# Kernel tuning notes

Measured on AMD Instinct MI355X. Metric: run time of the kernel, lower is better.

Reference implementation:

```python
import jax, jax.numpy as jnp
import numpy as np

N_NODES = 10000
N_EDGES = 160000
D = 512            # input_dim = hidden_size = output_dim
NUM_EXPERTS = 4
N_LAYERS = 2


def setup_inputs() -> dict:
    key = jax.random.key(0)
    k = jax.random.split(key, 7)
    x = jax.random.normal(k[0], (N_NODES, D), dtype=jnp.float32)
    edge_index = jax.random.randint(k[1], (2, N_EDGES), 0, N_NODES, dtype=jnp.int32)
    # Gating network (Linear D -> NUM_EXPERTS)
    gate_w = jax.random.normal(k[2], (D, NUM_EXPERTS), dtype=jnp.float32) * 0.05
    gate_b = jnp.zeros((NUM_EXPERTS,), dtype=jnp.float32)
    # Per-expert SAGEConv weights: lin_r (self/root) and lin_l (neighbor) + bias
    w_self = jax.random.normal(k[3], (NUM_EXPERTS, N_LAYERS, D, D), dtype=jnp.float32) * 0.05
    w_neigh = jax.random.normal(k[4], (NUM_EXPERTS, N_LAYERS, D, D), dtype=jnp.float32) * 0.05
    b_exp = jnp.zeros((NUM_EXPERTS, N_LAYERS, D), dtype=jnp.float32)
    return {"x": x, "edge_index": edge_index, "gate_w": gate_w, "gate_b": gate_b,
            "w_self": w_self, "w_neigh": w_neigh, "b_exp": b_exp, "top_k": 1}


def reference(x, edge_index, gate_w, gate_b, w_self, w_neigh, b_exp, top_k):
    n = x.shape[0]
    src, dst = edge_index[0], edge_index[1]
    # mean-aggregation normalization (PyG SAGEConv aggr='mean'); 0 for isolated nodes
    deg = jax.ops.segment_sum(jnp.ones_like(src, dtype=x.dtype), dst, num_segments=n)
    inv_deg = jnp.where(deg > 0, 1.0 / jnp.maximum(deg, 1.0), 0.0)[:, None]  # [N,1]

    # gating: softmax(Linear(x)) then top-k routing
    gate = jax.nn.softmax(x @ gate_w + gate_b, axis=-1)          # [N, E]
    top_vals, top_idx = jax.lax.top_k(gate, top_k)               # [N, k]

    def expert(ws, wn, b):  # ws, wn: [L, D, D]; b: [L, D]
        h = x
        for l in range(N_LAYERS):
            agg = jax.ops.segment_sum(h[src], dst, num_segments=n) * inv_deg
            # SAGEConv: lin_l(mean_neigh) + lin_r(x) + bias, then relu (norm='id', eval dropout)
            h = jax.nn.relu(agg @ wn[l] + h @ ws[l] + b[l])
        return h

    # dense all-expert compute (matches original module)
    outs = jax.vmap(expert)(w_self, w_neigh, b_exp)              # [E, N, D]
    outs = jnp.transpose(outs, (1, 0, 2))                        # [N, E, D]
    sel = jnp.take_along_axis(outs, top_idx[:, :, None], axis=1)  # [N, k, D]
    return jnp.sum(sel * top_vals[:, :, None], axis=1)           # [N, D]
```

## Files before the change

### kernel.cpp

```cpp
#include <hip/hip_runtime.h>
#include <hip/hip_bf16.h>
#include <cstdint>

#define N_NODES 10000
#define N_EDGES 160000
#define DIM 512
#define K1 1024
#define NEXP 4

typedef __bf16 bf16_t;
typedef bf16_t bf16x8 __attribute__((ext_vector_type(8)));
typedef float f32x4 __attribute__((ext_vector_type(4)));

#define AS1(p) ((__attribute__((address_space(1))) void*)(p))
#define AS3(p) ((__attribute__((address_space(3))) void*)(p))

__global__ void zero_kernel(int* __restrict__ deg, int* __restrict__ ecnt) {
    int i = blockIdx.x * blockDim.x + threadIdx.x;
    if (i < N_NODES) deg[i] = 0;
    if (i < NEXP) ecnt[i] = 0;
}

__global__ void gate_kernel(const float* __restrict__ x,
                            const float* __restrict__ gw,
                            const float* __restrict__ gb,
                            int* __restrict__ top_idx,
                            float* __restrict__ top_val,
                            bf16_t* __restrict__ acat) {
    const int wave = threadIdx.x >> 6;
    const int lane = threadIdx.x & 63;
    const int node = blockIdx.x * 4 + wave;
    if (node >= N_NODES) return;
    const float4* x4 = (const float4*)(x + (size_t)node * DIM);
    const float4* gw4 = (const float4*)gw;
    float4 xa = x4[lane * 2];
    float4 xb = x4[lane * 2 + 1];
    float xv[8] = { xa.x, xa.y, xa.z, xa.w, xb.x, xb.y, xb.z, xb.w };
    float a0 = 0.f, a1 = 0.f, a2 = 0.f, a3 = 0.f;
    #pragma unroll
    for (int c = 0; c < 8; c++) {
        float4 g = gw4[lane * 8 + c];
        a0 += xv[c] * g.x; a1 += xv[c] * g.y; a2 += xv[c] * g.z; a3 += xv[c] * g.w;
    }
    bf16x8 o;
    #pragma unroll
    for (int c = 0; c < 8; c++) o[c] = (bf16_t)xv[c];
    *(bf16x8*)(acat + (size_t)node * K1 + DIM + lane * 8) = o;
    for (int off = 32; off > 0; off >>= 1) {
        a0 += __shfl_xor(a0, off);
        a1 += __shfl_xor(a1, off);
        a2 += __shfl_xor(a2, off);
        a3 += __shfl_xor(a3, off);
    }
    if (lane == 0) {
        float z[4] = { a0 + gb[0], a1 + gb[1], a2 + gb[2], a3 + gb[3] };
        int bi = 0; float bm = z[0];
        for (int e = 1; e < 4; e++) if (z[e] > bm) { bm = z[e]; bi = e; }
        float den = 0.f;
        for (int e = 0; e < 4; e++) den += expf(z[e] - bm);
        top_idx[node] = bi;
        top_val[node] = 1.0f / den;
    }
}

__global__ void bucket_kernel(const int* __restrict__ top_idx,
                              int* __restrict__ ecnt,
                              int* __restrict__ lists) {
    __shared__ int lcnt[NEXP];
    __shared__ int base[NEXP];
    const int tid = threadIdx.x;
    if (tid < NEXP) lcnt[tid] = 0;
    __syncthreads();
    const int node = blockIdx.x * 256 + tid;
    int e = 0, rank = 0;
    if (node < N_NODES) {
        e = top_idx[node];
        rank = atomicAdd(&lcnt[e], 1);
    }
    __syncthreads();
    if (tid < NEXP) base[tid] = atomicAdd(&ecnt[tid], lcnt[tid]);
    __syncthreads();
    if (node < N_NODES) lists[e * N_NODES + base[e] + rank] = node;
}

__global__ void deg_kernel(const int* __restrict__ dst, int* __restrict__ deg) {
    int i = blockIdx.x * blockDim.x + threadIdx.x;
    if (i < N_EDGES) atomicAdd(&deg[dst[i]], 1);
}

__global__ void scan_kernel(const int* __restrict__ deg,
                            int* __restrict__ offs,
                            int* __restrict__ cursor) {
    __shared__ int wsum[16];
    __shared__ int carrysh;
    const int tid = threadIdx.x;
    const int lane = tid & 63;
    const int wv = tid >> 6;
    if (tid == 0) carrysh = 0;
    __syncthreads();
    for (int base = 0; base < N_NODES; base += 1024) {
        int i = base + tid;
        int v = (i < N_NODES) ? deg[i] : 0;
        int s = v;
        #pragma unroll
        for (int off = 1; off < 64; off <<= 1) {
            int t = __shfl_up(s, off);
            if (lane >= off) s += t;
        }
        if (lane == 63) wsum[wv] = s;
        int carry = carrysh;
        __syncthreads();
        if (wv == 0) {
            int w = (lane < 16) ? wsum[lane] : 0;
            #pragma unroll
            for (int off = 1; off < 16; off <<= 1) {
                int t = __shfl_up(w, off);
                if (lane >= off) w += t;
            }
            if (lane < 16) wsum[lane] = w;
        }
        __syncthreads();
        int wbase = (wv > 0) ? wsum[wv - 1] : 0;
        int excl = carry + wbase + s - v;
        if (i < N_NODES) { offs[i] = excl; cursor[i] = excl; }
        int total = wsum[15];
        __syncthreads();
        if (tid == 0) carrysh = carry + total;
        __syncthreads();
    }
    if (tid == 0) offs[N_NODES] = carrysh;
}

__global__ void fill_kernel(const int* __restrict__ src, const int* __restrict__ dst,
                            int* __restrict__ cursor, int* __restrict__ csr) {
    int i = blockIdx.x * blockDim.x + threadIdx.x;
    if (i < N_EDGES) {
        int d = dst[i];
        int p = atomicAdd(&cursor[d], 1);
        csr[p] = src[i];
    }
}

__global__ void wtrans_kernel(const float* __restrict__ w_neigh,
                              const float* __restrict__ w_self,
                              bf16_t* __restrict__ Bt) {
    __shared__ float tile[32][33];
    const int m = blockIdx.z;
    const bool isSelf = m >= 8;
    const int el = m & 7;
    const float* W = (isSelf ? w_self : w_neigh) + (size_t)el * DIM * DIM;
    const int k0 = blockIdx.x * 32;
    const int n0 = blockIdx.y * 32;
    const int tx = threadIdx.x, ty = threadIdx.y;
    for (int r = ty; r < 32; r += 8)
        tile[r][tx] = W[(size_t)(k0 + r) * DIM + n0 + tx];
    __syncthreads();
    for (int r = ty; r < 32; r += 8) {
        int n = n0 + r;
        int k = k0 + tx;
        Bt[((size_t)el * DIM + n) * K1 + (isSelf ? DIM : 0) + k] = (bf16_t)tile[tx][r];
    }
}

__global__ void agg1_kernel(const int* __restrict__ offs, const int* __restrict__ csr,
                            bf16_t* __restrict__ acat) {
    const int wave = threadIdx.x >> 6;
    const int lane = threadIdx.x & 63;
    const int node = blockIdx.x * 4 + wave;
    if (node >= N_NODES) return;
    const int c0 = lane * 8;
    float s[8] = {0,0,0,0,0,0,0,0};
    int beg = offs[node];
    int end = offs[node + 1];
    int d = end - beg;
    int p = beg;
    for (; p + 8 <= end; p += 8) {
        bf16x8 v[8];
        #pragma unroll
        for (int q = 0; q < 8; q++) {
            int idx = csr[p + q];
            v[q] = *(const bf16x8*)(acat + (size_t)idx * K1 + DIM + c0);
        }
        #pragma unroll
        for (int q = 0; q < 8; q++)
            #pragma unroll
            for (int k = 0; k < 8; k++) s[k] += (float)v[q][k];
    }
    for (; p + 4 <= end; p += 4) {
        bf16x8 v[4];
        #pragma unroll
        for (int q = 0; q < 4; q++) {
            int idx = csr[p + q];
            v[q] = *(const bf16x8*)(acat + (size_t)idx * K1 + DIM + c0);
        }
        #pragma unroll
        for (int q = 0; q < 4; q++)
            #pragma unroll
            for (int k = 0; k < 8; k++) s[k] += (float)v[q][k];
    }
    for (; p < end; p++) {
        int idx = csr[p];
        bf16x8 v0 = *(const bf16x8*)(acat + (size_t)idx * K1 + DIM + c0);
        #pragma unroll
        for (int k = 0; k < 8; k++) s[k] += (float)v0[k];
    }
    float w = d > 0 ? 1.0f / (float)d : 0.0f;
    bf16x8 o;
    #pragma unroll
    for (int k = 0; k < 8; k++) o[k] = (bf16_t)(s[k] * w);
    *(bf16x8*)(acat + (size_t)node * K1 + c0) = o;
}

__global__ void agg2_kernel(const int* __restrict__ offs, const int* __restrict__ csr,
                            const int* __restrict__ top_idx,
                            const bf16_t* __restrict__ h1, bf16_t* __restrict__ acat) {
    const int wave = threadIdx.x >> 6;
    const int lane = threadIdx.x & 63;
    const int node = blockIdx.x * 4 + wave;
    if (node >= N_NODES) return;
    const int c0 = lane * 8;
    const bf16_t* hb = h1 + (size_t)top_idx[node] * N_NODES * DIM;
    float s[8] = {0,0,0,0,0,0,0,0};
    int beg = offs[node];
    int end = offs[node + 1];
    int d = end - beg;
    int p = beg;
    for (; p + 8 <= end; p += 8) {
        bf16x8 v[8];
        #pragma unroll
        for (int q = 0; q < 8; q++) {
            int idx = csr[p + q];
            v[q] = *(const bf16x8*)(hb + (size_t)idx * DIM + c0);
        }
        #pragma unroll
        for (int q = 0; q < 8; q++)
            #pragma unroll
            for (int k = 0; k < 8; k++) s[k] += (float)v[q][k];
    }
    for (; p + 4 <= end; p += 4) {
        bf16x8 v[4];
        #pragma unroll
        for (int q = 0; q < 4; q++) {
            int idx = csr[p + q];
            v[q] = *(const bf16x8*)(hb + (size_t)idx * DIM + c0);
        }
        #pragma unroll
        for (int q = 0; q < 4; q++)
            #pragma unroll
            for (int k = 0; k < 8; k++) s[k] += (float)v[q][k];
    }
    for (; p < end; p++) {
        int idx = csr[p];
        bf16x8 v0 = *(const bf16x8*)(hb + (size_t)idx * DIM + c0);
        #pragma unroll
        for (int k = 0; k < 8; k++) s[k] += (float)v0[k];
    }
    float w = d > 0 ? 1.0f / (float)d : 0.0f;
    bf16x8 o;
    #pragma unroll
    for (int k = 0; k < 8; k++) o[k] = (bf16_t)(s[k] * w);
    *(bf16x8*)(acat + (size_t)node * K1 + c0) = o;
    *(bf16x8*)(acat + (size_t)node * K1 + DIM + c0) = *(const bf16x8*)(hb + (size_t)node * DIM + c0);
}

template <int MODE>
__global__ __launch_bounds__(256)
void gemm_kernel(const bf16_t* __restrict__ A,
                 const bf16_t* __restrict__ Bt,
                 const int layer,
                 const float* __restrict__ bias_all,
                 bf16_t* __restrict__ h1,
                 float* __restrict__ out,
                 const int* __restrict__ lists,
                 const int* __restrict__ ecnt,
                 const float* __restrict__ top_val) {
    int bx, by, e;
    if (MODE == 0) {
        const int b = blockIdx.x;
        const int kq = b & 7;
        const int ke = kq >> 2;
        const int ky = kq & 3;
        const int r = b >> 3;
        const int yloc = r >> 3;
        const int xz = r & 7;
        bx = xz & 3;
        e = ke * 2 + (xz >> 2);
        by = ky * 20 + yloc;
        if (by >= 79) return;
    } else {
        bx = blockIdx.x; by = blockIdx.y; e = blockIdx.z;
    }
    int cnt = N_NODES;
    if (MODE == 1) {
        cnt = ecnt[e];
        if (by * 128 >= cnt) return;
    }
    __shared__ __align__(16) bf16_t As[128 * 32];
    __shared__ __align__(16) bf16_t Bs[128 * 32];

    const int t = threadIdx.x;
    const int lane = t & 63;
    const int wave = t >> 6;
    const int wm = wave >> 1;
    const int wn = wave & 1;

    const int r0 = t >> 2;
    const int rot = (t >> 3) & 3;
    const int cgl = ((t & 3) - rot) & 3;

    int i0 = by * 128 + r0;
    int i1 = i0 + 64;
    int arow0, arow1;
    if (MODE == 0) {
        arow0 = min(i0, N_NODES - 1);
        arow1 = min(i1, N_NODES - 1);
    } else {
        arow0 = lists[e * N_NODES + min(i0, cnt - 1)];
        arow1 = lists[e * N_NODES + min(i1, cnt - 1)];
    }
    const bf16_t* Bte = Bt + (size_t)(e * 2 + layer) * DIM * K1;
    const bf16_t* aptr0 = A + (size_t)arow0 * K1 + cgl * 8;
    const bf16_t* aptr1 = A + (size_t)arow1 * K1 + cgl * 8;
    const bf16_t* bptr0 = Bte + (size_t)(bx * 128 + r0) * K1 + cgl * 8;
    const bf16_t* bptr1 = bptr0 + (size_t)64 * K1;

    f32x4 acc[4][4] = {};
    char* asb = (char*)&As[0];
    char* bsb = (char*)&Bs[0];
    const int wb = wave * 1024;

    const int cpr = lane >> 4;
    const int rfr = lane & 15;

    for (int k0 = 0; k0 < K1; k0 += 32) {
        __syncthreads();
        __builtin_amdgcn_global_load_lds(AS1(aptr0), AS3(asb + wb),        16, 0, 0);
        __builtin_amdgcn_global_load_lds(AS1(aptr1), AS3(asb + 4096 + wb), 16, 0, 0);
        __builtin_amdgcn_global_load_lds(AS1(bptr0), AS3(bsb + wb),        16, 0, 0);
        __builtin_amdgcn_global_load_lds(AS1(bptr1), AS3(bsb + 4096 + wb), 16, 0, 0);
        __syncthreads();
        bf16x8 af[4], bfr[4];
        #pragma unroll
        for (int i = 0; i < 4; i++) {
            int r_full = wm * 64 + i * 16 + rfr;
            int p = (cpr + (r_full >> 1)) & 3;
            af[i] = *(const bf16x8*)(As + r_full * 32 + p * 8);
        }
        #pragma unroll
        for (int j = 0; j < 4; j++) {
            int r_full = wn * 64 + j * 16 + rfr;
            int p = (cpr + (r_full >> 1)) & 3;
            bfr[j] = *(const bf16x8*)(Bs + r_full * 32 + p * 8);
        }
        #pragma unroll
        for (int i = 0; i < 4; i++)
            #pragma unroll
            for (int j = 0; j < 4; j++)
                acc[i][j] = __builtin_amdgcn_mfma_f32_16x16x32_bf16(af[i], bfr[j], acc[i][j], 0, 0, 0);
        aptr0 += 32; aptr1 += 32; bptr0 += 32; bptr1 += 32;
    }

    const float* bias = bias_all + e * 1024 + layer * DIM;
    const int cbase = bx * 128 + wn * 64 + (lane & 15);
    float bv[4];
    #pragma unroll
    for (int j = 0; j < 4; j++) bv[j] = bias[cbase + j * 16];
    #pragma unroll
    for (int i = 0; i < 4; i++) {
        #pragma unroll
        for (int r = 0; r < 4; r++) {
            int row = by * 128 + wm * 64 + i * 16 + (lane >> 4) * 4 + r;
            if (MODE == 0) {
                if (row < N_NODES) {
                    bf16_t* cp = h1 + ((size_t)e * N_NODES + row) * DIM + cbase;
                    #pragma unroll
                    for (int j = 0; j < 4; j++) {
                        float v = fmaxf(acc[i][j][r] + bv[j], 0.f);
                        cp[j * 16] = (bf16_t)v;
                    }
                }
            } else {
                if (row < cnt) {
                    int node = lists[e * N_NODES + row];
                    float tv = top_val[node];
                    float* cp = out + (size_t)node * DIM + cbase;
                    #pragma unroll
                    for (int j = 0; j < 4; j++) {
                        float v = fmaxf(acc[i][j][r] + bv[j], 0.f);
                        cp[j * 16] = v * tv;
                    }
                }
            }
        }
    }
}

extern "C" void kernel_launch(void* const* d_in, const int* in_sizes, int n_in,
                              void* d_out, int out_size, void* d_ws, size_t ws_size,
                              hipStream_t stream) {
    const float* x       = (const float*)d_in[0];
    const int*   edge    = (const int*)d_in[1];
    const float* gw      = (const float*)d_in[2];
    const float* gb      = (const float*)d_in[3];
    const float* w_self  = (const float*)d_in[4];
    const float* w_neigh = (const float*)d_in[5];
    const float* b_exp   = (const float*)d_in[6];
    float* out = (float*)d_out;

    char* p = (char*)d_ws;
    auto alloc = [&](size_t bytes) {
        char* r = p;
        p += (bytes + 255) & ~(size_t)255;
        return r;
    };
    bf16_t* Bt      = (bf16_t*)alloc((size_t)8 * DIM * K1 * 2);
    bf16_t* acat    = (bf16_t*)alloc((size_t)N_NODES * K1 * 2);
    bf16_t* h1      = (bf16_t*)alloc((size_t)NEXP * N_NODES * DIM * 2);
    int*    deg     = (int*)alloc((size_t)N_NODES * 4);
    int*    offs    = (int*)alloc((size_t)(N_NODES + 1) * 4);
    int*    cursor  = (int*)alloc((size_t)N_NODES * 4);
    int*    csr     = (int*)alloc((size_t)N_EDGES * 4);
    int*    top_idx = (int*)alloc((size_t)N_NODES * 4);
    float*  top_val = (float*)alloc((size_t)N_NODES * 4);
    int*    ecnt    = (int*)alloc(256);
    int*    lists   = (int*)alloc((size_t)NEXP * N_NODES * 4);

    const int* srcE = edge;
    const int* dstE = edge + N_EDGES;

    zero_kernel<<<40, 256, 0, stream>>>(deg, ecnt);
    gate_kernel<<<N_NODES / 4, 256, 0, stream>>>(x, gw, gb, top_idx, top_val, acat);
    bucket_kernel<<<40, 256, 0, stream>>>(top_idx, ecnt, lists);
    deg_kernel<<<N_EDGES / 256, 256, 0, stream>>>(dstE, deg);
    scan_kernel<<<1, 1024, 0, stream>>>(deg, offs, cursor);
    fill_kernel<<<N_EDGES / 256, 256, 0, stream>>>(srcE, dstE, cursor, csr);
    wtrans_kernel<<<dim3(16, 16, 16), dim3(32, 8), 0, stream>>>(w_neigh, w_self, Bt);
    agg1_kernel<<<N_NODES / 4, 256, 0, stream>>>(offs, csr, acat);
    gemm_kernel<0><<<1280, 256, 0, stream>>>(acat, Bt, 0, b_exp, h1, nullptr, nullptr, nullptr, nullptr);
    agg2_kernel<<<N_NODES / 4, 256, 0, stream>>>(offs, csr, top_idx, h1, acat);
    gemm_kernel<1><<<dim3(4, 79, 4), 256, 0, stream>>>(acat, Bt, 1, b_exp, nullptr, out, lists, ecnt, top_val);
}
```

Baseline: 280.4 us.

## Add dedicated layer-1 GEMM with 640x128 tiles and triple-buffered LDS pipeline

Replaces the generic layer-1 GEMM with a new kernel. It uses 512-thread blocks, each computing a 640-row by 128-column tile, so 256 blocks cover every node and all four experts' output columns. Operands move straight from global memory into LDS through three rotating buffers, with explicit vmcnt waits so loads overlap MFMA compute, and LDS reads use a swizzled layout. The larger tiles reuse each loaded row more, but need many accumulator registers (40 f32x4 per thread) and leave only 256 blocks, which risks low occupancy and poor load balance across CUs.

```diff
diff --git a/kernel.cpp b/kernel.cpp
--- a/kernel.cpp
+++ b/kernel.cpp
@@ -14,6 +14,8 @@
 
 #define AS1(p) ((__attribute__((address_space(1))) void*)(p))
 #define AS3(p) ((__attribute__((address_space(3))) void*)(p))
+
+#define VMW(N) asm volatile("s_waitcnt vmcnt(" #N ")" ::: "memory")
 
 __global__ void zero_kernel(int* __restrict__ deg, int* __restrict__ ecnt) {
     int i = blockIdx.x * blockDim.x + threadIdx.x;
@@ -261,6 +263,117 @@
     for (int k = 0; k < 8; k++) o[k] = (bf16_t)(s[k] * w);
     *(bf16x8*)(acat + (size_t)node * K1 + c0) = o;
     *(bf16x8*)(acat + (size_t)node * K1 + DIM + c0) = *(const bf16x8*)(hb + (size_t)node * DIM + c0);
+}
+
+__global__ __launch_bounds__(512, 2)
+void gemm_l1_kernel(const bf16_t* __restrict__ A,
+                    const bf16_t* __restrict__ Bt,
+                    const float* __restrict__ bias_all,
+                    bf16_t* __restrict__ h1) {
+    const int mtile = blockIdx.x >> 4;
+    const int ntile = blockIdx.x & 15;
+    const int e = ntile >> 2;
+
+    __shared__ __align__(16) bf16_t As[3 * 640 * 32];
+    __shared__ __align__(16) bf16_t Bs[3 * 128 * 32];
+
+    const int t = threadIdx.x;
+    const int lane = t & 63;
+    const int wave = t >> 6;
+    const int rloc = t >> 2;
+    const int cgl = ((t & 3) - ((t >> 3) & 3)) & 3;
+
+    const bf16_t* pA0 = A + (size_t)min(mtile * 640 +   0 + rloc, N_NODES - 1) * K1 + cgl * 8;
+    const bf16_t* pA1 = A + (size_t)min(mtile * 640 + 128 + rloc, N_NODES - 1) * K1 + cgl * 8;
+    const bf16_t* pA2 = A + (size_t)min(mtile * 640 + 256 + rloc, N_NODES - 1) * K1 + cgl * 8;
+    const bf16_t* pA3 = A + (size_t)min(mtile * 640 + 384 + rloc, N_NODES - 1) * K1 + cgl * 8;
+    const bf16_t* pA4 = A + (size_t)min(mtile * 640 + 512 + rloc, N_NODES - 1) * K1 + cgl * 8;
+    const bf16_t* pB0 = Bt + ((size_t)(e * 2 + 0) * DIM + (ntile & 3) * 128 + rloc) * K1 + cgl * 8;
+
+    char* asb = (char*)&As[0];
+    char* bsb = (char*)&Bs[0];
+
+    auto stage = [&](int bu) {
+        char* ab = asb + bu * 40960 + wave * 1024;
+        char* bb = bsb + bu * 8192  + wave * 1024;
+        __builtin_amdgcn_global_load_lds(AS1(pA0), AS3(ab),          16, 0, 0);
+        __builtin_amdgcn_global_load_lds(AS1(pA1), AS3(ab + 8192),   16, 0, 0);
+        __builtin_amdgcn_global_load_lds(AS1(pA2), AS3(ab + 16384),  16, 0, 0);
+        __builtin_amdgcn_global_load_lds(AS1(pA3), AS3(ab + 24576),  16, 0, 0);
+        __builtin_amdgcn_global_load_lds(AS1(pA4), AS3(ab + 32768),  16, 0, 0);
+        __builtin_amdgcn_global_load_lds(AS1(pB0), AS3(bb),          16, 0, 0);
+        pA0 += 32; pA1 += 32; pA2 += 32; pA3 += 32; pA4 += 32; pB0 += 32;
+    };
+
+    const int rfr = lane & 15;
+    const int cpr = lane >> 4;
+    const int wm = wave >> 1;
+    const int wn = wave & 1;
+    const int arow = wm * 160 + rfr;
+    const int brow = wn * 64 + rfr;
+    const int ppA = (cpr + (arow >> 1)) & 3;
+    const int ppB = (cpr + (brow >> 1)) & 3;
+    const int aoff = arow * 32 + ppA * 8;
+    const int boff = brow * 32 + ppB * 8;
+
+    f32x4 acc[10][4] = {};
+
+    auto compute = [&](int bu) {
+        const bf16_t* Ab = As + bu * 20480 + aoff;
+        const bf16_t* Bb = Bs + bu * 4096  + boff;
+        bf16x8 bfr[4];
+        #pragma unroll
+        for (int j = 0; j < 4; j++) bfr[j] = *(const bf16x8*)(Bb + j * 512);
+        #pragma unroll
+        for (int i = 0; i < 10; i++) {
+            bf16x8 af = *(const bf16x8*)(Ab + i * 512);
+            #pragma unroll
+            for (int j = 0; j < 4; j++)
+                acc[i][j] = __builtin_amdgcn_mfma_f32_16x16x32_bf16(af, bfr[j], acc[i][j], 0, 0, 0);
+        }
+    };
+
+    stage(0);
+    stage(1);
+
+    int cb = 0, sb = 2;
+    for (int tt = 0; tt < 31; ++tt) {
+        VMW(6);
+        __builtin_amdgcn_s_barrier();
+        asm volatile("" ::: "memory");
+        if (tt < 30) {
+            stage(sb);
+            sb = (sb == 2) ? 0 : sb + 1;
+        }
+        compute(cb);
+        cb = (cb == 2) ? 0 : cb + 1;
+    }
+    VMW(0);
+    __builtin_amdgcn_s_barrier();
+    asm volatile("" ::: "memory");
+    compute(cb);
+
+    const float* bias = bias_all + e * 1024;
+    const int cobase = (ntile & 3) * 128 + wn * 64 + (lane & 15);
+    float bv[4];
+    #pragma unroll
+    for (int j = 0; j < 4; j++) bv[j] = bias[cobase + j * 16];
+    const int rbase = mtile * 640 + wm * 160 + (lane >> 4) * 4;
+    #pragma unroll
+    for (int i = 0; i < 10; i++) {
+        #pragma unroll
+        for (int r = 0; r < 4; r++) {
+            int row = rbase + i * 16 + r;
+            if (row < N_NODES) {
+                bf16_t* cp = h1 + ((size_t)e * N_NODES + row) * DIM + cobase;
+                #pragma unroll
+                for (int j = 0; j < 4; j++) {
+                    float v = fmaxf(acc[i][j][r] + bv[j], 0.f);
+                    cp[j * 16] = (bf16_t)v;
+                }
+            }
+        }
+    }
 }
 
 template <int MODE>
@@ -436,7 +549,7 @@
     fill_kernel<<<N_EDGES / 256, 256, 0, stream>>>(srcE, dstE, cursor, csr);
     wtrans_kernel<<<dim3(16, 16, 16), dim3(32, 8), 0, stream>>>(w_neigh, w_self, Bt);
     agg1_kernel<<<N_NODES / 4, 256, 0, stream>>>(offs, csr, acat);
-    gemm_kernel<0><<<1280, 256, 0, stream>>>(acat, Bt, 0, b_exp, h1, nullptr, nullptr, nullptr, nullptr);
+    gemm_l1_kernel<<<256, 512, 0, stream>>>(acat, Bt, b_exp, h1);
     agg2_kernel<<<N_NODES / 4, 256, 0, stream>>>(offs, csr, top_idx, h1, acat);
     gemm_kernel<1><<<dim3(4, 79, 4), 256, 0, stream>>>(acat, Bt, 1, b_exp, nullptr, out, lists, ecnt, top_val);
 }
```

Result: slower. 287.1 us (+2.4%).
